# Kernel tuning notes

Measured on AMD Instinct MI355X. Metric: run time of the kernel, lower is better.

Reference implementation:

```python
import jax, jax.numpy as jnp
import numpy as np

B = 65536          # batch of response rows
R = 262144         # number of response rows
N_CELLS = 900
N_MISSING = 100
N_DRUGS = 256
NFEAT = 1024
CELL_EMB = 1024
DRUG_EMB = 128
HID = 200
NDOSES = 9


def setup_inputs() -> dict:
    key = jax.random.key(0)
    ks = jax.random.split(key, 16)
    inp = {
        "idx": jax.random.randint(ks[0], (B,), 0, R, dtype=jnp.int32),
        "tidx": jax.random.randint(ks[1], (B,), 0, R, dtype=jnp.int32),
        "is_missing": jax.random.randint(ks[2], (R,), 0, 2, dtype=jnp.int32),
        "cell_map": jax.random.randint(ks[3], (R,), 0, N_MISSING, dtype=jnp.int32),
        "drug_map": jax.random.randint(ks[4], (R,), 0, N_DRUGS, dtype=jnp.int32),
        "cell_features": jax.random.normal(ks[5], (N_CELLS, NFEAT), jnp.float32),
        "missing_emb": jax.random.normal(ks[6], (N_MISSING, CELL_EMB), jnp.float32) * 0.02,
        "drug_emb": jax.random.normal(ks[7], (N_DRUGS, DRUG_EMB), jnp.float32) * 0.02,
        "W1": jax.random.normal(ks[8], (NFEAT, CELL_EMB), jnp.float32) * 0.02,
        "b1": jax.random.normal(ks[9], (CELL_EMB,), jnp.float32) * 0.02,
        "Wf1": jax.random.normal(ks[10], (CELL_EMB + DRUG_EMB, HID), jnp.float32) * 0.02,
        "bf1": jax.random.normal(ks[11], (HID,), jnp.float32) * 0.02,
        "Wf2": jax.random.normal(ks[12], (HID, HID), jnp.float32) * 0.02,
        "bf2": jax.random.normal(ks[13], (HID,), jnp.float32) * 0.02,
        "Wf3": jax.random.normal(ks[14], (HID, NDOSES), jnp.float32) * 0.02,
        "bf3": jax.random.normal(ks[15], (NDOSES,), jnp.float32) * 0.02,
    }
    return inp


def _l2_normalize(x, eps=1e-12):
    # torch F.normalize: x / max(||x||_2, eps)
    n = jnp.sqrt(jnp.sum(x * x, axis=1, keepdims=True))
    return x / jnp.maximum(n, eps)


def reference(idx, tidx, is_missing, cell_map, drug_map, cell_features,
              missing_emb, drug_emb, W1, b1, Wf1, bf1, Wf2, bf2, Wf3, bf3):
    # --- cell_lookup, vectorized (eval mode: dropout = identity) ---
    cm = cell_map[idx]                                   # [B]
    miss = (is_missing[idx] != 0)[:, None]               # [B,1] bool
    feat = cell_features[cm]                             # [B, NFEAT]
    present = jax.nn.relu(feat @ W1 + b1)                # [B, CELL_EMB]
    missing = missing_emb[cm]                            # [B, CELL_EMB]
    cell_embeds = jnp.where(miss, missing, present)
    # --- drug_lookup ---
    drug_embeds = drug_emb[drug_map[tidx]]               # [B, DRUG_EMB]
    # --- embeds_to_predictions ---
    cell_embeds = _l2_normalize(cell_embeds)
    drug_embeds = _l2_normalize(drug_embeds)
    x = jnp.concatenate([cell_embeds, drug_embeds], axis=1)
    h = jax.nn.relu(x @ Wf1 + bf1)
    h = jax.nn.relu(h @ Wf2 + bf2)
    fwd = h @ Wf3 + bf3                                  # [B, NDOSES]
    base = fwd[:, 0:1]
    mu = jnp.concatenate(
        [base, base + jnp.cumsum(jax.nn.softplus(fwd[:, 1:]), axis=1)], axis=1)
    return mu  # [B, NDOSES + ... ] -> actually [B, 1 + (NDOSES-1) + 1]? No: [B, NDOSES]? see note
```

## Files before the change

### kernel.cpp

```cpp
#include <hip/hip_runtime.h>
#include <hip/hip_bf16.h>

#define NFEAT 1024
#define CELL_EMB 1024
#define DRUG_EMB 128
#define HID 200
#define NDOSES 9
#define N_MISSING 100
#define N_DRUGS 256
#define S 16
#define MUSTRIDE 12

typedef __hip_bfloat16 bf16;
typedef __attribute__((ext_vector_type(8))) short short8;
typedef __attribute__((ext_vector_type(4))) short short4v;
typedef __attribute__((ext_vector_type(4))) float float4v;

__device__ __forceinline__ float bf2f(short s) {
    unsigned u = ((unsigned)(unsigned short)s) << 16;
    return __builtin_bit_cast(float, u);
}
__device__ __forceinline__ short f2bf(float f) {
    unsigned u = __builtin_bit_cast(unsigned, f);
    unsigned r = (u + 0x7FFFu + ((u >> 16) & 1u)) >> 16;
    return (short)r;
}
template <bool F32>
__device__ __forceinline__ float ld(const void* p, int i) {
    if (F32) return ((const float*)p)[i];
    return bf2f(((const short*)p)[i]);
}
__device__ __forceinline__ float ldr(const void* p, int i, bool f32) {
    return f32 ? ((const float*)p)[i] : bf2f(((const short*)p)[i]);
}
__device__ __forceinline__ float softplusf(float x) {
    return (x > 20.f) ? x : log1pf(expf(x));
}


__global__ void sniff_k(const unsigned short* __restrict__ w, int* __restrict__ flag) {
    __shared__ int sf;
    if (threadIdx.x == 0) sf = 0;
    __syncthreads();
    int f = 0;
    for (int i = threadIdx.x; i < 4096; i += 256) {
        unsigned e = (w[i] >> 7) & 0xFFu;
        if (e >= 130u) f = 1;
    }
    if (f) atomicOr(&sf, 1);
    __syncthreads();
    if (threadIdx.x == 0) *flag = sf;
}

__global__ __launch_bounds__(256) void present_k(const int* __restrict__ flag,
                                                 const void* __restrict__ CF,
                                                 const void* __restrict__ W1,
                                                 const void* __restrict__ b1,
                                                 float* __restrict__ P) {
    __shared__ float feat[128];
    bool f32 = (*flag != 0);
    int c = blockIdx.x, kc = blockIdx.y, tid = threadIdx.x;
    if (tid < 128) feat[tid] = ldr(CF, c * NFEAT + kc * 128 + tid, f32);
    __syncthreads();
    int j0 = tid * 4;
    float a0 = 0.f, a1 = 0.f, a2 = 0.f, a3 = 0.f;
    if (f32) {
        const float* w = (const float*)W1 + (size_t)(kc * 128) * CELL_EMB + j0;
#pragma unroll 8
        for (int k = 0; k < 128; ++k) {
            float4v wv = *(const float4v*)(w + (size_t)k * CELL_EMB);
            float fk = feat[k];
            a0 = fmaf(fk, wv[0], a0); a1 = fmaf(fk, wv[1], a1);
            a2 = fmaf(fk, wv[2], a2); a3 = fmaf(fk, wv[3], a3);
        }
    } else {
        const short* w = (const short*)W1 + (size_t)(kc * 128) * CELL_EMB + j0;
#pragma unroll 8
        for (int k = 0; k < 128; ++k) {
            short4v wv = *(const short4v*)(w + (size_t)k * CELL_EMB);
            float fk = feat[k];
            a0 = fmaf(fk, bf2f(wv[0]), a0); a1 = fmaf(fk, bf2f(wv[1]), a1);
            a2 = fmaf(fk, bf2f(wv[2]), a2); a3 = fmaf(fk, bf2f(wv[3]), a3);
        }
    }
    if (kc == 0) {
        a0 += ldr(b1, j0 + 0, f32); a1 += ldr(b1, j0 + 1, f32);
        a2 += ldr(b1, j0 + 2, f32); a3 += ldr(b1, j0 + 3, f32);
    }
    float* pp = P + (size_t)c * CELL_EMB + j0;
    atomicAdd(pp + 0, a0); atomicAdd(pp + 1, a1);
    atomicAdd(pp + 2, a2); atomicAdd(pp + 3, a3);
}

__global__ __launch_bounds__(256) void norm_k(const int* __restrict__ flag,
                                              const float* __restrict__ P,
                                              const void* __restrict__ missing_emb,
                                              float* __restrict__ invC) {
    bool f32 = (*flag != 0);
    int r = blockIdx.x, tid = threadIdx.x;
    __shared__ float red[4];
    float4v v;
    if (r < N_MISSING) {
        v = ((const float4v*)(P + (size_t)r * CELL_EMB))[tid];
        v[0] = fmaxf(v[0], 0.f); v[1] = fmaxf(v[1], 0.f);
        v[2] = fmaxf(v[2], 0.f); v[3] = fmaxf(v[3], 0.f);
    } else if (f32) {
        v = ((const float4v*)((const float*)missing_emb + (size_t)(r - N_MISSING) * CELL_EMB))[tid];
    } else {
        short4v s = ((const short4v*)((const short*)missing_emb + (size_t)(r - N_MISSING) * CELL_EMB))[tid];
        v[0] = bf2f(s[0]); v[1] = bf2f(s[1]); v[2] = bf2f(s[2]); v[3] = bf2f(s[3]);
    }
    float ss = v[0] * v[0] + v[1] * v[1] + v[2] * v[2] + v[3] * v[3];
    for (int o = 32; o > 0; o >>= 1) ss += __shfl_down(ss, o, 64);
    if ((tid & 63) == 0) red[tid >> 6] = ss;
    __syncthreads();
    if (tid == 0)
        invC[r] = 1.f / fmaxf(sqrtf(red[0] + red[1] + red[2] + red[3]), 1e-12f);
}

__global__ __launch_bounds__(256) void cc_k(const int* __restrict__ flag,
                                            const float* __restrict__ P,
                                            const void* __restrict__ missing_emb,
                                            const float* __restrict__ invC,
                                            const void* __restrict__ Wf1,
                                            float* __restrict__ Cc) {
    __shared__ float x[128];
    bool f32 = (*flag != 0);
    int r = blockIdx.x, kc = blockIdx.y, tid = threadIdx.x;
    float inv = invC[r];
    if (tid < 128) {
        int k = kc * 128 + tid;
        float e = (r < N_MISSING)
                      ? fmaxf(P[(size_t)r * CELL_EMB + k], 0.f)
                      : ldr(missing_emb, (size_t)(r - N_MISSING) * CELL_EMB + k, f32);
        x[tid] = e * inv;
    }
    __syncthreads();
    if (tid < HID) {
        float acc = 0.f;
        if (f32) {
            const float* w = (const float*)Wf1 + (size_t)(kc * 128) * HID + tid;
#pragma unroll 8
            for (int k = 0; k < 128; ++k)
                acc = fmaf(x[k], w[(size_t)k * HID], acc);
        } else {
            const short* w = (const short*)Wf1 + (size_t)(kc * 128) * HID + tid;
#pragma unroll 8
            for (int k = 0; k < 128; ++k)
                acc = fmaf(x[k], bf2f(w[(size_t)k * HID]), acc);
        }
        atomicAdd(&Cc[r * HID + tid], acc);
    }
}

__global__ __launch_bounds__(256) void dc_k(const int* __restrict__ flag,
                                            const void* __restrict__ drug_emb,
                                            const void* __restrict__ Wf1,
                                            float* __restrict__ Dc) {
    bool f32 = (*flag != 0);
    int d = blockIdx.x, tid = threadIdx.x;
    __shared__ float x[DRUG_EMB];
    __shared__ float red[4];
    if (tid < DRUG_EMB) x[tid] = ldr(drug_emb, d * DRUG_EMB + tid, f32);
    __syncthreads();
    float ss = 0.f;
    if (tid < DRUG_EMB) ss = x[tid] * x[tid];
    for (int o = 32; o > 0; o >>= 1) ss += __shfl_down(ss, o, 64);
    if ((tid & 63) == 0) red[tid >> 6] = ss;
    __syncthreads();
    float inv = 1.f / fmaxf(sqrtf(red[0] + red[1] + red[2] + red[3]), 1e-12f);
    if (tid < HID) {
        float acc = 0.f;
#pragma unroll 8
        for (int k = 0; k < DRUG_EMB; ++k)
            acc = fmaf(x[k], ldr(Wf1, (CELL_EMB + k) * HID + tid, f32), acc);
        Dc[d * HID + tid] = acc * inv;
    }
}

#define KSTEPS 7
#define NTP 7

__global__ __launch_bounds__(64) void prepb_k(const int* __restrict__ flag,
                                              const void* __restrict__ Wf2,
                                              short8* __restrict__ Bf) {
    bool f32 = (*flag != 0);
    int t = blockIdx.x * 64 + threadIdx.x;
    int l = t & 63, chunk = t >> 6;
    int p = chunk / 49, rem = chunk - p * 49;
    int nt = rem / 7, s = rem - nt * 7;
    int n = p * 112 + nt * 16 + (l & 15);
    int k0 = s * 32 + (l >> 4) * 8;
    short8 v;
#pragma unroll
    for (int j = 0; j < 8; ++j) {
        int k = k0 + j;
        v[j] = (k < HID && n < HID) ? f2bf(ldr(Wf2, k * HID + n, f32)) : (short)0;
    }
    Bf[t] = v;
}

#define KP 224
#define MB 64

__global__ __launch_bounds__(256) void pair_k(const int* __restrict__ flag,
                                              const float* __restrict__ Cc,
                                              const float* __restrict__ Dc,
                                              const void* __restrict__ bf1,
                                              const void* __restrict__ bf2,
                                              const void* __restrict__ Wf3,
                                              const short8* __restrict__ Bf,
                                              float* __restrict__ mu) {
    __shared__ float Crow[KP];
    __shared__ float bf2s[KP];
    __shared__ short wf3s[KP * NDOSES];
    bool f32 = (*flag != 0);
    int tid = threadIdx.x;
    int lane = tid & 63, w = tid >> 6;
    int q = lane >> 4, col = lane & 15;
    int r0 = blockIdx.x * MB;
    int c = r0 >> 8;
    int d0 = r0 & 255;

    for (int k = tid; k < KP; k += 256) {
        Crow[k] = (k < HID) ? Cc[c * HID + k] + ldr(bf1, k, f32) : 0.f;
        bf2s[k] = (k < HID) ? ldr(bf2, k, f32) : 0.f;
    }
    for (int t = tid; t < KP * NDOSES; t += 256) {
        int k = t / NDOSES, dd = t - k * NDOSES;
        wf3s[t] = (k < HID) ? f2bf(ldr(Wf3, k * NDOSES + dd, f32)) : (short)0;
    }
    __syncthreads();

    int arow = d0 + w * 16 + col;

    short8 a[KSTEPS];
#pragma unroll
    for (int s = 0; s < KSTEPS; ++s) {
        int k0 = s * 32 + q * 8;
        if (k0 < HID) {
            float4v c0 = *(const float4v*)(&Crow[k0]);
            float4v c1 = *(const float4v*)(&Crow[k0 + 4]);
            float4v dv0 = *(const float4v*)(Dc + (size_t)arow * HID + k0);
            float4v dv1 = *(const float4v*)(Dc + (size_t)arow * HID + k0 + 4);
#pragma unroll
            for (int j = 0; j < 4; ++j) {
                a[s][j]     = f2bf(fmaxf(c0[j] + dv0[j], 0.f));
                a[s][j + 4] = f2bf(fmaxf(c1[j] + dv1[j], 0.f));
            }
        } else {
#pragma unroll
            for (int j = 0; j < 8; ++j) a[s][j] = 0;
        }
    }

    float fw[4][9];
#pragma unroll
    for (int i = 0; i < 4; ++i)
#pragma unroll
        for (int dd = 0; dd < 9; ++dd) fw[i][dd] = 0.f;

    for (int p = 0; p < 2; ++p) {
        float4v acc[NTP];
#pragma unroll
        for (int nt = 0; nt < NTP; ++nt) acc[nt] = 0.f;
#pragma unroll
        for (int s = 0; s < KSTEPS; ++s) {
#pragma unroll
            for (int nt = 0; nt < NTP; ++nt) {
                short8 bb = Bf[(size_t)((p * 7 + nt) * 7 + s) * 64 + lane];
                acc[nt] = __builtin_amdgcn_mfma_f32_16x16x32_bf16(a[s], bb, acc[nt], 0, 0, 0);
            }
        }
#pragma unroll
        for (int nt = 0; nt < NTP; ++nt) {
            int n = p * 112 + nt * 16 + col;
            float bb2 = bf2s[n];
            float w3[9];
#pragma unroll
            for (int dd = 0; dd < 9; ++dd) w3[dd] = bf2f(wf3s[n * NDOSES + dd]);
#pragma unroll
            for (int rg = 0; rg < 4; ++rg) {
                float h2 = fmaxf(acc[nt][rg] + bb2, 0.f);
#pragma unroll
                for (int dd = 0; dd < 9; ++dd)
                    fw[rg][dd] = fmaf(h2, w3[dd], fw[rg][dd]);
            }
        }
    }
#pragma unroll
    for (int i = 0; i < 4; ++i)
#pragma unroll
        for (int dd = 0; dd < 9; ++dd) {
            float v = fw[i][dd];
            v += __shfl_xor(v, 1, 16);
            v += __shfl_xor(v, 2, 16);
            v += __shfl_xor(v, 4, 16);
            v += __shfl_xor(v, 8, 16);
            fw[i][dd] = v;
        }
#pragma unroll
    for (int i = 0; i < 4; ++i) {
        int row = r0 + w * 16 + q * 4 + i;
        float myval = 0.f;
#pragma unroll
        for (int dd = 0; dd < 9; ++dd) myval = (col == dd) ? fw[i][dd] : myval;
        float v = (col == 0) ? myval : softplusf(myval);
        float t1 = __shfl_up(v, 1, 16); if (col >= 1) v += t1;
        float t2 = __shfl_up(v, 2, 16); if (col >= 2) v += t2;
        float t4 = __shfl_up(v, 4, 16); if (col >= 4) v += t4;
        float t8 = __shfl_up(v, 8, 16); if (col >= 8) v += t8;
        if (col < NDOSES) mu[(size_t)row * MUSTRIDE + col] = v;
    }
}

__global__ __launch_bounds__(256) void gather_k(const int* __restrict__ flag,
                                                const int* __restrict__ idx,
                                                const int* __restrict__ tidx,
                                                const int* __restrict__ is_missing,
                                                const int* __restrict__ cell_map,
                                                const int* __restrict__ drug_map,
                                                const float* __restrict__ mu,
                                                void* __restrict__ out, int nB) {
    int b = blockIdx.x * 256 + threadIdx.x;
    if (b >= nB) return;
    bool f32 = (*flag != 0);
    int i = idx[b];
    int cm = cell_map[i];
    int kc = (is_missing[i] != 0) ? (N_MISSING + cm) : cm;
    int kd = drug_map[tidx[b]];
    const float* mr = mu + (size_t)(kc * 256 + kd) * MUSTRIDE;
    float4v m0 = *(const float4v*)mr;
    float4v m1 = *(const float4v*)(mr + 4);
    float m8 = mr[8];
    float vals[9] = {m0[0], m0[1], m0[2], m0[3], m1[0], m1[1], m1[2], m1[3], m8};
    if (f32) {
        float* o = (float*)out + (size_t)b * NDOSES;
#pragma unroll
        for (int dd = 0; dd < 9; ++dd) o[dd] = vals[dd];
    } else {
        short* o = (short*)out + (size_t)b * NDOSES;
#pragma unroll
        for (int dd = 0; dd < 9; ++dd) o[dd] = f2bf(vals[dd]);
    }
}


__global__ void sniff_kernel(const unsigned short* __restrict__ w1bits, int* __restrict__ flag) {
    if (threadIdx.x == 0 && blockIdx.x == 0) {
        int f = 0;
        for (int i = 0; i < 512; ++i) {
            unsigned int e = (w1bits[i] >> 7) & 0xFFu;
            if (e >= 130u) f = 1;
        }
        *flag = f;
    }
}

template <bool F32>
__global__ __launch_bounds__(256) void present_kernel(const int* __restrict__ flag,
                                                      const void* __restrict__ cell_features,
                                                      const void* __restrict__ W1,
                                                      const void* __restrict__ b1,
                                                      float* __restrict__ P) {
    if (*flag != (int)F32) return;
    __shared__ float feat[NFEAT];
    int c = blockIdx.x, jb = blockIdx.y;
    for (int k = threadIdx.x; k < NFEAT; k += 256)
        feat[k] = ld<F32>(cell_features, c * NFEAT + k);
    __syncthreads();
    int j = jb * 256 + threadIdx.x;
    float acc = ld<F32>(b1, j);
    for (int k = 0; k < NFEAT; ++k)
        acc = fmaf(feat[k], ld<F32>(W1, k * CELL_EMB + j), acc);
    P[c * CELL_EMB + j] = fmaxf(acc, 0.f);
}

template <bool F32>
__global__ __launch_bounds__(256) void cc_kernel(const int* __restrict__ flag,
                                                 const float* __restrict__ P,
                                                 const void* __restrict__ missing_emb,
                                                 const void* __restrict__ Wf1,
                                                 float* __restrict__ Cc) {
    if (*flag != (int)F32) return;
    int r = blockIdx.x;
    __shared__ float x[CELL_EMB];
    __shared__ float red[4];
    if (r < N_MISSING) {
        for (int k = threadIdx.x; k < CELL_EMB; k += 256) x[k] = P[r * CELL_EMB + k];
    } else {
        for (int k = threadIdx.x; k < CELL_EMB; k += 256)
            x[k] = ld<F32>(missing_emb, (r - N_MISSING) * CELL_EMB + k);
    }
    __syncthreads();
    float ss = 0.f;
    for (int k = threadIdx.x; k < CELL_EMB; k += 256) ss += x[k] * x[k];
    for (int o = 32; o > 0; o >>= 1) ss += __shfl_down(ss, o, 64);
    if ((threadIdx.x & 63) == 0) red[threadIdx.x >> 6] = ss;
    __syncthreads();
    float inv = 1.f / fmaxf(sqrtf(red[0] + red[1] + red[2] + red[3]), 1e-12f);
    int j = threadIdx.x;
    if (j < HID) {
        float acc = 0.f;
        for (int k = 0; k < CELL_EMB; ++k)
            acc = fmaf(x[k], ld<F32>(Wf1, k * HID + j), acc);
        Cc[r * HID + j] = acc * inv;
    }
}

template <bool F32>
__global__ __launch_bounds__(256) void dc_kernel(const int* __restrict__ flag,
                                                 const void* __restrict__ drug_emb,
                                                 const void* __restrict__ Wf1,
                                                 float* __restrict__ Dc) {
    if (*flag != (int)F32) return;
    int d = blockIdx.x;
    __shared__ float x[DRUG_EMB];
    __shared__ float red[4];
    if (threadIdx.x < DRUG_EMB) x[threadIdx.x] = ld<F32>(drug_emb, d * DRUG_EMB + threadIdx.x);
    __syncthreads();
    float ss = 0.f;
    if (threadIdx.x < DRUG_EMB) ss = x[threadIdx.x] * x[threadIdx.x];
    for (int o = 32; o > 0; o >>= 1) ss += __shfl_down(ss, o, 64);
    if ((threadIdx.x & 63) == 0) red[threadIdx.x >> 6] = ss;
    __syncthreads();
    float inv = 1.f / fmaxf(sqrtf(red[0] + red[1] + red[2] + red[3]), 1e-12f);
    int j = threadIdx.x;
    if (j < HID) {
        float acc = 0.f;
        for (int k = 0; k < DRUG_EMB; ++k)
            acc = fmaf(x[k], ld<F32>(Wf1, (CELL_EMB + k) * HID + j), acc);
        Dc[d * HID + j] = acc * inv;
    }
}

template <bool F32>
__global__ __launch_bounds__(256) void main_kernel(const int* __restrict__ flag,
                                                   const int* __restrict__ idx,
                                                   const int* __restrict__ tidx,
                                                   const int* __restrict__ is_missing,
                                                   const int* __restrict__ cell_map,
                                                   const int* __restrict__ drug_map,
                                                   const float* __restrict__ Cc,
                                                   const float* __restrict__ Dc,
                                                   const void* __restrict__ bf1,
                                                   const void* __restrict__ Wf2,
                                                   const void* __restrict__ bf2,
                                                   const void* __restrict__ Wf3,
                                                   const void* __restrict__ bf3,
                                                   void* __restrict__ out, int nB) {
    if (*flag != (int)F32) return;
    __shared__ float h1t[HID][S];
    __shared__ float h2[S][HID];
    __shared__ float wf3s[HID * NDOSES];
    __shared__ float bf3s[NDOSES];
    __shared__ int keyc[S], keyd[S];
    __shared__ float fwds[S][NDOSES];

    int b0 = blockIdx.x * S;
    int tid = threadIdx.x;

    if (tid < S) {
        int b = b0 + tid;
        if (b < nB) {
            int i = idx[b];
            int cm = cell_map[i];
            keyc[tid] = (is_missing[i] != 0) ? (N_MISSING + cm) : cm;
            keyd[tid] = drug_map[tidx[b]];
        } else { keyc[tid] = 0; keyd[tid] = 0; }
    }
    for (int t = tid; t < HID * NDOSES; t += 256) wf3s[t] = ld<F32>(Wf3, t);
    if (tid < NDOSES) bf3s[tid] = ld<F32>(bf3, tid);
    __syncthreads();

    for (int t = tid; t < S * HID; t += 256) {
        int s = t / HID;
        int j = t - s * HID;
        float v = Cc[keyc[s] * HID + j] + Dc[keyd[s] * HID + j] + ld<F32>(bf1, j);
        h1t[j][s] = fmaxf(v, 0.f);
    }
    __syncthreads();

    if (tid < HID) {
        float acc[S];
#pragma unroll
        for (int s = 0; s < S; ++s) acc[s] = 0.f;
        for (int i = 0; i < HID; ++i) {
            float wv = ld<F32>(Wf2, i * HID + tid);
#pragma unroll
            for (int s = 0; s < S; ++s) acc[s] = fmaf(h1t[i][s], wv, acc[s]);
        }
        float bb = ld<F32>(bf2, tid);
#pragma unroll
        for (int s = 0; s < S; ++s) h2[s][tid] = fmaxf(acc[s] + bb, 0.f);
    }
    __syncthreads();

    if (tid < S * NDOSES) {
        int s = tid / NDOSES;
        int k = tid - s * NDOSES;
        float acc = bf3s[k];
        for (int j = 0; j < HID; ++j)
            acc = fmaf(h2[s][j], wf3s[j * NDOSES + k], acc);
        fwds[s][k] = acc;
    }
    __syncthreads();

    if (tid < S && b0 + tid < nB) {
        float m = fwds[tid][0];
        long o = (long)(b0 + tid) * NDOSES;
        if (F32) ((float*)out)[o] = m; else ((short*)out)[o] = f2bf(m);
#pragma unroll
        for (int k = 1; k < NDOSES; ++k) {
            float x = fwds[tid][k];
            m += softplusf(x);
            if (F32) ((float*)out)[o + k] = m;
            else     ((short*)out)[o + k] = f2bf(m);
        }
    }
}


extern "C" void kernel_launch(void* const* d_in, const int* in_sizes, int n_in,
                              void* d_out, int out_size, void* d_ws, size_t ws_size,
                              hipStream_t stream) {
    const int* idx        = (const int*)d_in[0];
    const int* tidx       = (const int*)d_in[1];
    const int* is_missing = (const int*)d_in[2];
    const int* cell_map   = (const int*)d_in[3];
    const int* drug_map   = (const int*)d_in[4];
    const void* CF   = d_in[5];
    const void* memb = d_in[6];
    const void* demb = d_in[7];
    const void* W1   = d_in[8];
    const void* b1   = d_in[9];
    const void* Wf1  = d_in[10];
    const void* bf1v = d_in[11];
    const void* Wf2  = d_in[12];
    const void* bf2v = d_in[13];
    const void* Wf3  = d_in[14];
    const void* bf3v = d_in[15];

    int nB = in_sizes[0];
    const size_t NEED = 731008ull * 4ull;

    if (ws_size >= NEED) {
        float* ws   = (float*)d_ws;
        int*   flag = (int*)d_ws;
        float* Cc   = ws + 64;
        float* invC = ws + 40064;
        float* Dc   = ws + 40320;
        float* Bf   = ws + 91520;
        float* mu   = ws + 116608;
        float* P    = mu;

        hipMemsetAsync(P, 0, 102400 * sizeof(float), stream);
        hipMemsetAsync(Cc, 0, 40000 * sizeof(float), stream);
        hipLaunchKernelGGL(sniff_k, dim3(1), dim3(256), 0, stream,
                           (const unsigned short*)W1, flag);
        hipLaunchKernelGGL(present_k, dim3(N_MISSING, 8), dim3(256), 0, stream,
                           flag, CF, W1, b1, P);
        hipLaunchKernelGGL(norm_k, dim3(2 * N_MISSING), dim3(256), 0, stream,
                           flag, P, memb, invC);
        hipLaunchKernelGGL(cc_k, dim3(2 * N_MISSING, 8), dim3(256), 0, stream,
                           flag, P, memb, invC, Wf1, Cc);
        hipLaunchKernelGGL(dc_k, dim3(N_DRUGS), dim3(256), 0, stream,
                           flag, demb, Wf1, Dc);
        hipLaunchKernelGGL(prepb_k, dim3(98), dim3(64), 0, stream,
                           flag, Wf2, (short8*)Bf);
        hipLaunchKernelGGL(pair_k, dim3(800), dim3(256), 0, stream,
                           flag, Cc, Dc, bf1v, bf2v, Wf3, (const short8*)Bf, mu);
        hipLaunchKernelGGL(gather_k, dim3((nB + 255) / 256), dim3(256), 0, stream,
                           flag, idx, tidx, is_missing, cell_map, drug_map, mu, d_out, nB);
    } else {
        float* ws   = (float*)d_ws;
        int*   flag = (int*)d_ws;
        float* P    = ws + 64;
        float* Cc   = P + 102400;
        float* Dc   = Cc + 40000;

        hipLaunchKernelGGL(sniff_kernel, dim3(1), dim3(64), 0, stream,
                           (const unsigned short*)W1, flag);
#define LAUNCH_BOTH(name, grid, blk, ...)                                          \
        hipLaunchKernelGGL((name<false>), grid, blk, 0, stream, flag, __VA_ARGS__);\
        hipLaunchKernelGGL((name<true>),  grid, blk, 0, stream, flag, __VA_ARGS__);
        LAUNCH_BOTH(present_kernel, dim3(N_MISSING, 4), dim3(256), CF, W1, b1, P)
        LAUNCH_BOTH(cc_kernel, dim3(2 * N_MISSING), dim3(256), P, memb, Wf1, Cc)
        LAUNCH_BOTH(dc_kernel, dim3(N_DRUGS), dim3(256), demb, Wf1, Dc)
        LAUNCH_BOTH(main_kernel, dim3((nB + S - 1) / S), dim3(256),
                    idx, tidx, is_missing, cell_map, drug_map, Cc, Dc,
                    bf1v, Wf2, bf2v, Wf3, bf3v, d_out, nB)
#undef LAUNCH_BOTH
    }
}
```

Baseline: 190.6 us.

## Merge prep kernels into one launch and inline dtype sniffing per kernel

Result: faster. 162.1 us (-15.0%).

```diff
diff --git a/kernel.cpp b/kernel.cpp
--- a/kernel.cpp
+++ b/kernel.cpp
@@ -37,105 +37,141 @@
     return (x > 20.f) ? x : log1pf(expf(x));
 }
 
-
-__global__ void sniff_k(const unsigned short* __restrict__ w, int* __restrict__ flag) {
-    __shared__ int sf;
-    if (threadIdx.x == 0) sf = 0;
-    __syncthreads();
-    int f = 0;
-    for (int i = threadIdx.x; i < 4096; i += 256) {
-        unsigned e = (w[i] >> 7) & 0xFFu;
-        if (e >= 130u) f = 1;
-    }
-    if (f) atomicOr(&sf, 1);
-    __syncthreads();
-    if (threadIdx.x == 0) *flag = sf;
-}
-
-__global__ __launch_bounds__(256) void present_k(const int* __restrict__ flag,
-                                                 const void* __restrict__ CF,
-                                                 const void* __restrict__ W1,
-                                                 const void* __restrict__ b1,
-                                                 float* __restrict__ P) {
-    __shared__ float feat[128];
-    bool f32 = (*flag != 0);
-    int c = blockIdx.x, kc = blockIdx.y, tid = threadIdx.x;
-    if (tid < 128) feat[tid] = ldr(CF, c * NFEAT + kc * 128 + tid, f32);
-    __syncthreads();
-    int j0 = tid * 4;
-    float a0 = 0.f, a1 = 0.f, a2 = 0.f, a3 = 0.f;
-    if (f32) {
-        const float* w = (const float*)W1 + (size_t)(kc * 128) * CELL_EMB + j0;
+__device__ __forceinline__ bool sniff_f32(const unsigned short* __restrict__ w1) {
+    int lane = threadIdx.x & 63;
+    unsigned short h = w1[lane];
+    bool hit = ((lane & 1) == 0) && (((h >> 7) & 0xFFu) >= 130u);
+    return __ballot(hit) != 0ull;
+}
+
+
+#define GP_PRESENT 800
+#define GP_DC_END (GP_PRESENT + 256)
+#define GP_PB_END (GP_DC_END + 25)
+#define GP_CZ_END (GP_PB_END + 40)
+
+__global__ __launch_bounds__(256) void mega_prep_k(const void* __restrict__ CF,
+                                                   const unsigned short* __restrict__ W1u,
+                                                   const void* __restrict__ b1,
+                                                   const void* __restrict__ drug_emb,
+                                                   const void* __restrict__ Wf1,
+                                                   const void* __restrict__ Wf2,
+                                                   float* __restrict__ P8,
+                                                   float* __restrict__ Dc,
+                                                   short8* __restrict__ Bf,
+                                                   float* __restrict__ Cc) {
+    bool f32 = sniff_f32(W1u);
+    const void* W1 = (const void*)W1u;
+    int blk = blockIdx.x, tid = threadIdx.x;
+
+    if (blk < GP_PRESENT) {
+        __shared__ float feat[128];
+        int c = blk >> 3, kc = blk & 7;
+        if (tid < 128) feat[tid] = ldr(CF, c * NFEAT + kc * 128 + tid, f32);
+        __syncthreads();
+        int j0 = tid * 4;
+        float a0 = 0.f, a1 = 0.f, a2 = 0.f, a3 = 0.f;
+        if (f32) {
+            const float* w = (const float*)W1 + (size_t)(kc * 128) * CELL_EMB + j0;
 #pragma unroll 8
-        for (int k = 0; k < 128; ++k) {
-            float4v wv = *(const float4v*)(w + (size_t)k * CELL_EMB);
-            float fk = feat[k];
-            a0 = fmaf(fk, wv[0], a0); a1 = fmaf(fk, wv[1], a1);
-            a2 = fmaf(fk, wv[2], a2); a3 = fmaf(fk, wv[3], a3);
+            for (int k = 0; k < 128; ++k) {
+                float4v wv = *(const float4v*)(w + (size_t)k * CELL_EMB);
+                float fk = feat[k];
+                a0 = fmaf(fk, wv[0], a0); a1 = fmaf(fk, wv[1], a1);
+                a2 = fmaf(fk, wv[2], a2); a3 = fmaf(fk, wv[3], a3);
+            }
+        } else {
+            const short* w = (const short*)W1 + (size_t)(kc * 128) * CELL_EMB + j0;
+#pragma unroll 8
+            for (int k = 0; k < 128; ++k) {
+                short4v wv = *(const short4v*)(w + (size_t)k * CELL_EMB);
+                float fk = feat[k];
+                a0 = fmaf(fk, bf2f(wv[0]), a0); a1 = fmaf(fk, bf2f(wv[1]), a1);
+                a2 = fmaf(fk, bf2f(wv[2]), a2); a3 = fmaf(fk, bf2f(wv[3]), a3);
+            }
+        }
+        if (kc == 0) {
+            a0 += ldr(b1, j0 + 0, f32); a1 += ldr(b1, j0 + 1, f32);
+            a2 += ldr(b1, j0 + 2, f32); a3 += ldr(b1, j0 + 3, f32);
+        }
+        float4v o; o[0] = a0; o[1] = a1; o[2] = a2; o[3] = a3;
+        *(float4v*)(P8 + ((size_t)(kc * N_MISSING + c)) * CELL_EMB + j0) = o;
+    } else if (blk < GP_DC_END) {
+        __shared__ float x[DRUG_EMB];
+        __shared__ float red[4];
+        int d = blk - GP_PRESENT;
+        if (tid < DRUG_EMB) x[tid] = ldr(drug_emb, d * DRUG_EMB + tid, f32);
+        __syncthreads();
+        float ss = 0.f;
+        if (tid < DRUG_EMB) ss = x[tid] * x[tid];
+        for (int o = 32; o > 0; o >>= 1) ss += __shfl_down(ss, o, 64);
+        if ((tid & 63) == 0) red[tid >> 6] = ss;
+        __syncthreads();
+        float inv = 1.f / fmaxf(sqrtf(red[0] + red[1] + red[2] + red[3]), 1e-12f);
+        if (tid < HID) {
+            float acc = 0.f;
+#pragma unroll 8
+            for (int k = 0; k < DRUG_EMB; ++k)
+                acc = fmaf(x[k], ldr(Wf1, (CELL_EMB + k) * HID + tid, f32), acc);
+            Dc[d * HID + tid] = acc * inv;
+        }
+    } else if (blk < GP_PB_END) {
+        int t = (blk - GP_DC_END) * 256 + tid;
+        if (t < 6272) {
+            int l = t & 63, chunk = t >> 6;
+            int p = chunk / 49, rem = chunk - p * 49;
+            int nt = rem / 7, s = rem - nt * 7;
+            int n = p * 112 + nt * 16 + (l & 15);
+            int k0 = s * 32 + (l >> 4) * 8;
+            short8 v;
+#pragma unroll
+            for (int j = 0; j < 8; ++j) {
+                int k = k0 + j;
+                v[j] = (k < HID && n < HID) ? f2bf(ldr(Wf2, k * HID + n, f32)) : (short)0;
+            }
+            Bf[t] = v;
         }
     } else {
-        const short* w = (const short*)W1 + (size_t)(kc * 128) * CELL_EMB + j0;
-#pragma unroll 8
-        for (int k = 0; k < 128; ++k) {
-            short4v wv = *(const short4v*)(w + (size_t)k * CELL_EMB);
-            float fk = feat[k];
-            a0 = fmaf(fk, bf2f(wv[0]), a0); a1 = fmaf(fk, bf2f(wv[1]), a1);
-            a2 = fmaf(fk, bf2f(wv[2]), a2); a3 = fmaf(fk, bf2f(wv[3]), a3);
-        }
-    }
-    if (kc == 0) {
-        a0 += ldr(b1, j0 + 0, f32); a1 += ldr(b1, j0 + 1, f32);
-        a2 += ldr(b1, j0 + 2, f32); a3 += ldr(b1, j0 + 3, f32);
-    }
-    float* pp = P + (size_t)c * CELL_EMB + j0;
-    atomicAdd(pp + 0, a0); atomicAdd(pp + 1, a1);
-    atomicAdd(pp + 2, a2); atomicAdd(pp + 3, a3);
-}
-
-__global__ __launch_bounds__(256) void norm_k(const int* __restrict__ flag,
-                                              const float* __restrict__ P,
-                                              const void* __restrict__ missing_emb,
-                                              float* __restrict__ invC) {
-    bool f32 = (*flag != 0);
-    int r = blockIdx.x, tid = threadIdx.x;
+        int i = (blk - GP_PB_END) * 1024 + tid * 4;
+        if (i < 200 * HID) {
+            float4v z; z[0] = 0.f; z[1] = 0.f; z[2] = 0.f; z[3] = 0.f;
+            *(float4v*)(Cc + i) = z;
+        }
+    }
+}
+
+__global__ __launch_bounds__(256) void cc_k(const unsigned short* __restrict__ W1u,
+                                            const float* __restrict__ P8,
+                                            const void* __restrict__ missing_emb,
+                                            const void* __restrict__ Wf1,
+                                            float* __restrict__ Cc) {
+    __shared__ __align__(16) float x[128];
     __shared__ float red[4];
+    bool f32 = sniff_f32(W1u);
+    int r = blockIdx.x, kc = blockIdx.y, tid = threadIdx.x;
+    int e0 = tid * 4;
     float4v v;
     if (r < N_MISSING) {
-        v = ((const float4v*)(P + (size_t)r * CELL_EMB))[tid];
+        v[0] = 0.f; v[1] = 0.f; v[2] = 0.f; v[3] = 0.f;
+#pragma unroll
+        for (int p = 0; p < 8; ++p) {
+            float4v t = *(const float4v*)(P8 + ((size_t)(p * N_MISSING + r)) * CELL_EMB + e0);
+            v[0] += t[0]; v[1] += t[1]; v[2] += t[2]; v[3] += t[3];
+        }
         v[0] = fmaxf(v[0], 0.f); v[1] = fmaxf(v[1], 0.f);
         v[2] = fmaxf(v[2], 0.f); v[3] = fmaxf(v[3], 0.f);
     } else if (f32) {
-        v = ((const float4v*)((const float*)missing_emb + (size_t)(r - N_MISSING) * CELL_EMB))[tid];
+        v = *(const float4v*)((const float*)missing_emb + (size_t)(r - N_MISSING) * CELL_EMB + e0);
     } else {
-        short4v s = ((const short4v*)((const short*)missing_emb + (size_t)(r - N_MISSING) * CELL_EMB))[tid];
+        short4v s = *(const short4v*)((const short*)missing_emb + (size_t)(r - N_MISSING) * CELL_EMB + e0);
         v[0] = bf2f(s[0]); v[1] = bf2f(s[1]); v[2] = bf2f(s[2]); v[3] = bf2f(s[3]);
     }
+    if ((tid >> 5) == kc) *(float4v*)(x + (e0 - kc * 128)) = v;
     float ss = v[0] * v[0] + v[1] * v[1] + v[2] * v[2] + v[3] * v[3];
     for (int o = 32; o > 0; o >>= 1) ss += __shfl_down(ss, o, 64);
     if ((tid & 63) == 0) red[tid >> 6] = ss;
     __syncthreads();
-    if (tid == 0)
-        invC[r] = 1.f / fmaxf(sqrtf(red[0] + red[1] + red[2] + red[3]), 1e-12f);
-}
-
-__global__ __launch_bounds__(256) void cc_k(const int* __restrict__ flag,
-                                            const float* __restrict__ P,
-                                            const void* __restrict__ missing_emb,
-                                            const float* __restrict__ invC,
-                                            const void* __restrict__ Wf1,
-                                            float* __restrict__ Cc) {
-    __shared__ float x[128];
-    bool f32 = (*flag != 0);
-    int r = blockIdx.x, kc = blockIdx.y, tid = threadIdx.x;
-    float inv = invC[r];
-    if (tid < 128) {
-        int k = kc * 128 + tid;
-        float e = (r < N_MISSING)
-                      ? fmaxf(P[(size_t)r * CELL_EMB + k], 0.f)
-                      : ldr(missing_emb, (size_t)(r - N_MISSING) * CELL_EMB + k, f32);
-        x[tid] = e * inv;
-    }
-    __syncthreads();
+    float inv = 1.f / fmaxf(sqrtf(red[0] + red[1] + red[2] + red[3]), 1e-12f);
     if (tid < HID) {
         float acc = 0.f;
         if (f32) {
@@ -149,61 +185,16 @@
             for (int k = 0; k < 128; ++k)
                 acc = fmaf(x[k], bf2f(w[(size_t)k * HID]), acc);
         }
-        atomicAdd(&Cc[r * HID + tid], acc);
-    }
-}
-
-__global__ __launch_bounds__(256) void dc_k(const int* __restrict__ flag,
-                                            const void* __restrict__ drug_emb,
-                                            const void* __restrict__ Wf1,
-                                            float* __restrict__ Dc) {
-    bool f32 = (*flag != 0);
-    int d = blockIdx.x, tid = threadIdx.x;
-    __shared__ float x[DRUG_EMB];
-    __shared__ float red[4];
-    if (tid < DRUG_EMB) x[tid] = ldr(drug_emb, d * DRUG_EMB + tid, f32);
-    __syncthreads();
-    float ss = 0.f;
-    if (tid < DRUG_EMB) ss = x[tid] * x[tid];
-    for (int o = 32; o > 0; o >>= 1) ss += __shfl_down(ss, o, 64);
-    if ((tid & 63) == 0) red[tid >> 6] = ss;
-    __syncthreads();
-    float inv = 1.f / fmaxf(sqrtf(red[0] + red[1] + red[2] + red[3]), 1e-12f);
-    if (tid < HID) {
-        float acc = 0.f;
-#pragma unroll 8
-        for (int k = 0; k < DRUG_EMB; ++k)
-            acc = fmaf(x[k], ldr(Wf1, (CELL_EMB + k) * HID + tid, f32), acc);
-        Dc[d * HID + tid] = acc * inv;
+        atomicAdd(&Cc[r * HID + tid], acc * inv);
     }
 }
 
 #define KSTEPS 7
 #define NTP 7
-
-__global__ __launch_bounds__(64) void prepb_k(const int* __restrict__ flag,
-                                              const void* __restrict__ Wf2,
-                                              short8* __restrict__ Bf) {
-    bool f32 = (*flag != 0);
-    int t = blockIdx.x * 64 + threadIdx.x;
-    int l = t & 63, chunk = t >> 6;
-    int p = chunk / 49, rem = chunk - p * 49;
-    int nt = rem / 7, s = rem - nt * 7;
-    int n = p * 112 + nt * 16 + (l & 15);
-    int k0 = s * 32 + (l >> 4) * 8;
-    short8 v;
-#pragma unroll
-    for (int j = 0; j < 8; ++j) {
-        int k = k0 + j;
-        v[j] = (k < HID && n < HID) ? f2bf(ldr(Wf2, k * HID + n, f32)) : (short)0;
-    }
-    Bf[t] = v;
-}
-
 #define KP 224
 #define MB 64
 
-__global__ __launch_bounds__(256) void pair_k(const int* __restrict__ flag,
+__global__ __launch_bounds__(256) void pair_k(const unsigned short* __restrict__ W1u,
                                               const float* __restrict__ Cc,
                                               const float* __restrict__ Dc,
                                               const void* __restrict__ bf1,
@@ -214,7 +205,7 @@
     __shared__ float Crow[KP];
     __shared__ float bf2s[KP];
     __shared__ short wf3s[KP * NDOSES];
-    bool f32 = (*flag != 0);
+    bool f32 = sniff_f32(W1u);
     int tid = threadIdx.x;
     int lane = tid & 63, w = tid >> 6;
     int q = lane >> 4, col = lane & 15;
@@ -314,7 +305,7 @@
     }
 }
 
-__global__ __launch_bounds__(256) void gather_k(const int* __restrict__ flag,
+__global__ __launch_bounds__(256) void gather_k(const unsigned short* __restrict__ W1u,
                                                 const int* __restrict__ idx,
                                                 const int* __restrict__ tidx,
                                                 const int* __restrict__ is_missing,
@@ -322,9 +313,9 @@
                                                 const int* __restrict__ drug_map,
                                                 const float* __restrict__ mu,
                                                 void* __restrict__ out, int nB) {
+    bool f32 = sniff_f32(W1u);
     int b = blockIdx.x * 256 + threadIdx.x;
     if (b >= nB) return;
-    bool f32 = (*flag != 0);
     int i = idx[b];
     int cm = cell_map[i];
     int kc = (is_missing[i] != 0) ? (N_MISSING + cm) : cm;
@@ -542,36 +533,27 @@
     const void* bf3v = d_in[15];
 
     int nB = in_sizes[0];
-    const size_t NEED = 731008ull * 4ull;
+    const size_t NEED = 935552ull * 4ull;
 
     if (ws_size >= NEED) {
         float* ws   = (float*)d_ws;
-        int*   flag = (int*)d_ws;
         float* Cc   = ws + 64;
-        float* invC = ws + 40064;
-        float* Dc   = ws + 40320;
-        float* Bf   = ws + 91520;
-        float* mu   = ws + 116608;
-        float* P    = mu;
-
-        hipMemsetAsync(P, 0, 102400 * sizeof(float), stream);
-        hipMemsetAsync(Cc, 0, 40000 * sizeof(float), stream);
-        hipLaunchKernelGGL(sniff_k, dim3(1), dim3(256), 0, stream,
-                           (const unsigned short*)W1, flag);
-        hipLaunchKernelGGL(present_k, dim3(N_MISSING, 8), dim3(256), 0, stream,
-                           flag, CF, W1, b1, P);
-        hipLaunchKernelGGL(norm_k, dim3(2 * N_MISSING), dim3(256), 0, stream,
-                           flag, P, memb, invC);
+        float* Dc   = ws + 40064;
+        float* Bf   = ws + 91264;
+        float* P8   = ws + 116352;
+        float* mu   = P8;
+
+        hipLaunchKernelGGL(mega_prep_k, dim3(GP_CZ_END), dim3(256), 0, stream,
+                           CF, (const unsigned short*)W1, b1, demb, Wf1, Wf2,
+                           P8, Dc, (short8*)Bf, Cc);
         hipLaunchKernelGGL(cc_k, dim3(2 * N_MISSING, 8), dim3(256), 0, stream,
-                           flag, P, memb, invC, Wf1, Cc);
-        hipLaunchKernelGGL(dc_k, dim3(N_DRUGS), dim3(256), 0, stream,
-                           flag, demb, Wf1, Dc);
-        hipLaunchKernelGGL(prepb_k, dim3(98), dim3(64), 0, stream,
-                           flag, Wf2, (short8*)Bf);
+                           (const unsigned short*)W1, P8, memb, Wf1, Cc);
         hipLaunchKernelGGL(pair_k, dim3(800), dim3(256), 0, stream,
-                           flag, Cc, Dc, bf1v, bf2v, Wf3, (const short8*)Bf, mu);
+                           (const unsigned short*)W1, Cc, Dc, bf1v, bf2v, Wf3,
+                           (const short8*)Bf, mu);
         hipLaunchKernelGGL(gather_k, dim3((nB + 255) / 256), dim3(256), 0, stream,
-                           flag, idx, tidx, is_missing, cell_map, drug_map, mu, d_out, nB);
+                           (const unsigned short*)W1, idx, tidx, is_missing,
+                           cell_map, drug_map, mu, d_out, nB);
     } else {
         float* ws   = (float*)d_ws;
         int*   flag = (int*)d_ws;
```
